# Performance work log

Hardware: AMD Instinct MI355X
Metric: run time of the kernel (lower is better)

## Reference

```python
import jax, jax.numpy as jnp
import numpy as np

B, T, E, H, M = 1, 2048, 1536, 16, 3
KVH = 8
NREP = H // KVH
HD = E // H // M  # 32
EPS = 1e-5


def setup_inputs() -> dict:
    key = jax.random.key(0)
    ks = jax.random.split(key, 6)
    x = jax.random.normal(ks[0], (B, T, E), jnp.float32)
    # true rotary tables: freqs = pos * 10000^{-2i/d}, shape [T, HD//2]
    inv_freq = 1.0 / (10000.0 ** (np.arange(0, HD, 2, dtype=np.float64) / HD))
    ang = np.outer(np.arange(T, dtype=np.float64), inv_freq)
    cos = jnp.asarray(np.cos(ang), jnp.float32)
    sin = jnp.asarray(np.sin(ang), jnp.float32)
    s = 0.02
    q_w = s * jax.random.normal(ks[1], (M, E // M, E), jnp.float32)
    k_w = s * jax.random.normal(ks[2], (M, E // M // NREP, E), jnp.float32)
    v_w = s * jax.random.normal(ks[3], (E // NREP, E), jnp.float32)
    out_w = s * jax.random.normal(ks[4], (E, E), jnp.float32)
    raw_map_weights = jnp.array([0.1, -0.1, 0.1], jnp.float32)
    weight_scale = jnp.ones((1,), jnp.float32)
    subln_w = jnp.ones((M * HD,), jnp.float32)
    return dict(x=x, cos=cos, sin=sin, q_w=q_w, k_w=k_w, v_w=v_w,
                out_w=out_w, raw_map_weights=raw_map_weights,
                weight_scale=weight_scale, subln_w=subln_w)


def _rope_interleaved(t, cos, sin):
    # t: [..., seq, heads, hd]; cos/sin: [seq, hd//2]
    x1 = t[..., 0::2]
    x2 = t[..., 1::2]
    c = cos[:, None, :]
    s = sin[:, None, :]
    o1 = x1 * c - x2 * s
    o2 = x1 * s + x2 * c
    return jnp.stack([o1, o2], axis=-1).reshape(t.shape)


def reference(x, cos, sin, q_w, k_w, v_w, out_w, raw_map_weights, weight_scale, subln_w):
    b, t, e = x.shape
    m = q_w.shape[0]
    hd = 2 * cos.shape[-1]
    h = q_w.shape[1] // hd
    kvh = k_w.shape[1] // hd
    nrep = h // kvh
    scaling = hd ** -0.5

    map_w = jnp.tanh(raw_map_weights) * weight_scale  # [M]

    # per-map Q/K projections, all maps at once
    q = jnp.einsum('bte,mfe->mbtf', x, q_w).reshape(m, b, t, h, hd)
    k = jnp.einsum('bte,mfe->mbtf', x, k_w).reshape(m, b, t, kvh, hd)
    q = _rope_interleaved(q, cos, sin) * scaling
    k = _rope_interleaved(k, cos, sin)
    q = q.transpose(0, 1, 3, 2, 4)                      # [m,b,h,t,hd]
    k = jnp.repeat(k.transpose(0, 1, 3, 2, 4), nrep, axis=2)  # [m,b,h,t,hd]

    v = jnp.einsum('bte,fe->btf', x, v_w).reshape(b, t, kvh, m * hd)
    v = jnp.repeat(v.transpose(0, 2, 1, 3), nrep, axis=1)  # [b,h,t,m*hd]

    causal = jnp.where(jnp.triu(jnp.ones((t, t), bool), 1),
                       jnp.float32(-jnp.inf), jnp.float32(0.0))

    scores = jnp.einsum('mbhtd,mbhsd->mbhts', q, k)
    scores = jnp.nan_to_num(scores) + causal
    attn_w = jax.nn.softmax(scores.astype(jnp.float32), axis=-1).astype(x.dtype)
    combined = jnp.einsum('m,mbhts->bhts', map_w, attn_w)

    attn = jnp.einsum('bhts,bhsf->bhtf', combined, v)  # [b,h,t,m*hd]
    # RMSNorm over last dim
    var = jnp.mean(jnp.square(attn.astype(jnp.float32)), axis=-1, keepdims=True)
    attn = (attn * jax.lax.rsqrt(var + EPS)).astype(attn.dtype) * subln_w

    attn = attn.transpose(0, 2, 1, 3).reshape(b, t, h * m * hd)
    return jnp.einsum('bte,fe->btf', attn, out_w)
```

## Files before the change

kernel.cpp:

```cpp
#include <hip/hip_runtime.h>
#include <hip/hip_bf16.h>
#include <math.h>

#define T_DIM 2048
#define E_DIM 1536
#define K_DIM 1536

typedef unsigned short u16;
typedef unsigned int u32;
typedef __attribute__((ext_vector_type(8))) short bf16x8;
typedef __attribute__((ext_vector_type(4))) float f32x4;

__device__ __forceinline__ u16 f2bf(float x) {
    unsigned u = __float_as_uint(x);
    return (u16)((u + 0x7fffu + ((u >> 16) & 1u)) >> 16);
}

#define GLOAD16(gsrc, ldst)                                                              \
    __builtin_amdgcn_global_load_lds((const __attribute__((address_space(1))) u32*)(gsrc), \
                                     (__attribute__((address_space(3))) u32*)(ldst), 16, 0, 0)

__global__ __launch_bounds__(256) void cvt_bf16_5(const float* __restrict__ s0, u16* __restrict__ d0,
                                                  const float* __restrict__ s1, u16* __restrict__ d1,
                                                  const float* __restrict__ s2, u16* __restrict__ d2,
                                                  const float* __restrict__ s3, u16* __restrict__ d3,
                                                  const float* __restrict__ s4, u16* __restrict__ d4) {
    int i = blockIdx.x * 256 + threadIdx.x;
    const float* s;
    u16* d;
    int off;
    if (i < 786432)       { s = s0; d = d0; off = i; }
    else if (i < 1376256) { s = s1; d = d1; off = i - 786432; }
    else if (i < 1671168) { s = s2; d = d2; off = i - 1376256; }
    else if (i < 1966080) { s = s3; d = d3; off = i - 1671168; }
    else                  { s = s4; d = d4; off = i - 1966080; }
    float4 v = ((const float4*)s)[off];
    ((ushort4*)d)[off] = make_ushort4(f2bf(v.x), f2bf(v.y), f2bf(v.z), f2bf(v.w));
}

__global__ __launch_bounds__(256) void gemm_qkv_fused(const u16* __restrict__ A,
                                                      const u16* __restrict__ W,
                                                      const float* __restrict__ cosb,
                                                      const float* __restrict__ sinb,
                                                      u16* __restrict__ qb16,
                                                      u16* __restrict__ kpack,
                                                      u16* __restrict__ vpack,
                                                      float qscale) {
    const int K = K_DIM;
    __shared__ __align__(16) u16 As[128 * 64];
    __shared__ __align__(16) u16 Bs[128 * 64];
    const int tid = threadIdx.x;
    const int lane = tid & 63;
    const int wv = tid >> 6;
    const int wr = wv >> 1;
    const int wc = wv & 1;
    const int cl = lane & 15;
    const int g = lane >> 4;
    const int bm = blockIdx.y * 128;
    const int bn = blockIdx.x * 128;

    const char* Ab = (const char*)A;
    const char* Wb = (const char*)W;

    size_t a_src[4], b_src[4];
    int dst[4];
#pragma unroll
    for (int is = 0; is < 4; ++is) {
        int b = is * 4096 + tid * 16;
        int row = b >> 7;
        int wi = b & 127;
        dst[is] = b;
        a_src[is] = (size_t)(bm + row) * (K * 2) + (wi ^ ((row & 7) << 4));
        b_src[is] = (size_t)(bn + row) * (K * 2) + (wi ^ ((row & 7) << 4));
    }

    f32x4 acc[4][4];
#pragma unroll
    for (int mi = 0; mi < 4; ++mi)
#pragma unroll
        for (int ni = 0; ni < 4; ++ni) acc[mi][ni] = (f32x4){0.f, 0.f, 0.f, 0.f};

    for (int k0b = 0; k0b < K * 2; k0b += 128) {
#pragma unroll
        for (int is = 0; is < 4; ++is)
            GLOAD16(Ab + a_src[is] + k0b, (char*)As + dst[is]);
#pragma unroll
        for (int is = 0; is < 4; ++is)
            GLOAD16(Wb + b_src[is] + k0b, (char*)Bs + dst[is]);
        __syncthreads();
#pragma unroll
        for (int kk = 0; kk < 2; ++kk) {
            const int co = (kk * 64 + g * 16) ^ ((cl & 7) << 4);
            bf16x8 af[4], bfr[4];
#pragma unroll
            for (int mi = 0; mi < 4; ++mi)
                af[mi] = *(const bf16x8*)((const char*)As + (wr * 64 + mi * 16 + cl) * 128 + co);
#pragma unroll
            for (int ni = 0; ni < 4; ++ni)
                bfr[ni] = *(const bf16x8*)((const char*)Bs + (wc * 64 + ni * 16 + cl) * 128 + co);
#pragma unroll
            for (int mi = 0; mi < 4; ++mi)
#pragma unroll
                for (int ni = 0; ni < 4; ++ni)
                    acc[mi][ni] = __builtin_amdgcn_mfma_f32_16x16x32_bf16(af[mi], bfr[ni], acc[mi][ni], 0, 0, 0);
        }
        __syncthreads();
    }

    if (bn < 1536) {
#pragma unroll
        for (int mi = 0; mi < 4; ++mi)
#pragma unroll
            for (int ni = 0; ni < 4; ++ni)
#pragma unroll
                for (int r = 0; r < 4; ++r) {
                    int trow = bm + wr * 64 + mi * 16 + 4 * g + r;
                    int c = bn + wc * 64 + ni * 16 + cl;
                    float v = acc[mi][ni][r];
                    float pv = __shfl_xor(v, 1, 64);
                    int i = (c & 31) >> 1;
                    float cs = cosb[trow * 16 + i];
                    float sn = sinb[trow * 16 + i];
                    float o = v * cs + ((c & 1) ? pv * sn : -pv * sn);
                    qb16[(size_t)trow * E_DIM + c] = f2bf(o * qscale);
                }
    } else if (bn < 2304) {
#pragma unroll
        for (int mi = 0; mi < 4; ++mi)
#pragma unroll
            for (int ni = 0; ni < 4; ++ni)
#pragma unroll
                for (int r = 0; r < 4; ++r) {
                    int trow = bm + wr * 64 + mi * 16 + 4 * g + r;
                    int c = bn + wc * 64 + ni * 16 + cl;
                    float v = acc[mi][ni][r];
                    float pv = __shfl_xor(v, 1, 64);
                    int i = (c & 31) >> 1;
                    float cs = cosb[trow * 16 + i];
                    float sn = sinb[trow * 16 + i];
                    float o = v * cs + ((c & 1) ? pv * sn : -pv * sn);
                    int ck = c - 1536;
                    int m = ck >> 8;
                    int rem = ck & 255;
                    int kvhh = rem >> 5;
                    int d = rem & 31;
                    int cch = trow >> 5, st2 = (trow >> 4) & 1, colk = trow & 15;
                    size_t dstb = ((((size_t)(kvhh * 64 + cch) * 3 + m) * 2 + st2) * 16 + colk) * 32 + d;
                    kpack[dstb] = f2bf(o);
                }
    } else {
#pragma unroll
        for (int mi = 0; mi < 4; ++mi)
#pragma unroll
            for (int ni = 0; ni < 4; ++ni)
#pragma unroll
                for (int r = 0; r < 4; ++r) {
                    int trow = bm + wr * 64 + mi * 16 + 4 * g + r;
                    int c = bn + wc * 64 + ni * 16 + cl;
                    int fq = c - 2304;
                    int kvhh = fq / 96;
                    int f = fq - kvhh * 96;
                    size_t dstb = ((size_t)(kvhh * 64 + (trow >> 5)) * 96 + f) * 32 + (trow & 31);
                    vpack[dstb] = f2bf(acc[mi][ni][r]);
                }
    }
}

__global__ __launch_bounds__(256) void gemm_mfma_out(const u16* __restrict__ A,
                                                     const u16* __restrict__ W,
                                                     float* __restrict__ Cp,
                                                     int K, int ldC) {
    __shared__ __align__(16) u16 As[128 * 64];
    __shared__ __align__(16) u16 Bs[64 * 64];
    const int tid = threadIdx.x;
    const int lane = tid & 63;
    const int wv = tid >> 6;
    const int wr = wv >> 1;
    const int wc = wv & 1;
    const int cl = lane & 15;
    const int g = lane >> 4;
    const int bm = blockIdx.y * 128;
    const int bn = blockIdx.x * 64;

    const char* Ab = (const char*)A;
    const char* Wb = (const char*)W;

    size_t a_src[4];
    int a_dst[4];
#pragma unroll
    for (int is = 0; is < 4; ++is) {
        int b = is * 4096 + wv * 1024 + lane * 16;
        int row = b >> 7;
        int wi = b & 127;
        a_src[is] = (size_t)(bm + row) * (K * 2) + (wi ^ ((row & 7) << 4));
        a_dst[is] = b;
    }
    size_t b_src[2];
    int b_dst[2];
#pragma unroll
    for (int is = 0; is < 2; ++is) {
        int b = is * 4096 + wv * 1024 + lane * 16;
        int row = b >> 7;
        int wi = b & 127;
        b_src[is] = (size_t)(bn + row) * (K * 2) + (wi ^ ((row & 7) << 4));
        b_dst[is] = b;
    }

    f32x4 acc[4][2];
#pragma unroll
    for (int mi = 0; mi < 4; ++mi)
#pragma unroll
        for (int ni = 0; ni < 2; ++ni) acc[mi][ni] = (f32x4){0.f, 0.f, 0.f, 0.f};

    for (int k0b = 0; k0b < K * 2; k0b += 128) {
#pragma unroll
        for (int is = 0; is < 4; ++is)
            GLOAD16(Ab + a_src[is] + k0b, (char*)As + a_dst[is]);
#pragma unroll
        for (int is = 0; is < 2; ++is)
            GLOAD16(Wb + b_src[is] + k0b, (char*)Bs + b_dst[is]);
        __syncthreads();
#pragma unroll
        for (int kk = 0; kk < 2; ++kk) {
            const int co = (kk * 64 + g * 16) ^ ((cl & 7) << 4);
            bf16x8 af[4], bfr[2];
#pragma unroll
            for (int mi = 0; mi < 4; ++mi)
                af[mi] = *(const bf16x8*)((const char*)As + (wr * 64 + mi * 16 + cl) * 128 + co);
#pragma unroll
            for (int ni = 0; ni < 2; ++ni)
                bfr[ni] = *(const bf16x8*)((const char*)Bs + (wc * 32 + ni * 16 + cl) * 128 + co);
#pragma unroll
            for (int mi = 0; mi < 4; ++mi)
#pragma unroll
                for (int ni = 0; ni < 2; ++ni)
                    acc[mi][ni] = __builtin_amdgcn_mfma_f32_16x16x32_bf16(af[mi], bfr[ni], acc[mi][ni], 0, 0, 0);
        }
        __syncthreads();
    }

#pragma unroll
    for (int mi = 0; mi < 4; ++mi)
#pragma unroll
        for (int ni = 0; ni < 2; ++ni)
#pragma unroll
            for (int r = 0; r < 4; ++r) {
                size_t row = bm + wr * 64 + mi * 16 + 4 * g + r;
                size_t col = bn + wc * 32 + ni * 16 + cl;
                Cp[row * ldC + col] = acc[mi][ni][r];
            }
}

__global__ __launch_bounds__(384) void attn_one(const u16* __restrict__ qb,
                                                const u16* __restrict__ kpack,
                                                const u16* __restrict__ vpack,
                                                const float* __restrict__ raw_map,
                                                const float* __restrict__ wscale,
                                                const float* __restrict__ subln,
                                                u16* __restrict__ outb) {
    __shared__ __align__(16) char smem[36864];
    const int tid = threadIdx.x;
    const int lane = tid & 63;
    const int wv = tid >> 6;
    const int m = wv >> 1;
    const int ks = wv & 1;
    const int col = lane & 15;
    const int g = lane >> 4;
    const int lid = blockIdx.y * 64 + blockIdx.x;
    const int kvh = lid & 7;
    const int rest = lid >> 3;
    const int h = kvh * 2 + (rest & 1);
    const int qt = 63 - (rest >> 1);
    const int qbase = qt * 32;
    const int nfull = qt;

    u16 (*plds)[2][16][48] = (u16(*)[2][16][48])smem;
    float (*red1)[2][16] = (float(*)[2][16])smem;

    bf16x8 qfrag[2];
#pragma unroll
    for (int q2 = 0; q2 < 2; ++q2)
        qfrag[q2] = *(const bf16x8*)(qb + (size_t)(qbase + 16 * q2 + col) * E_DIM + m * 512 + h * 32 + 8 * g);

    f32x4 oacc[2][6];
#pragma unroll
    for (int q2 = 0; q2 < 2; ++q2)
#pragma unroll
        for (int ft = 0; ft < 6; ++ft) oacc[q2][ft] = (f32x4){0.f, 0.f, 0.f, 0.f};
    float lsum[2] = {0.f, 0.f};

    const int laneoff = col * 32 + 8 * g;
    const u16* kt = kpack + ((size_t)(kvh * 64 + ks) * 3 + m) * 1024 + laneoff;
    const u16* vt = vpack + (size_t)(kvh * 64 + ks) * 3072 + laneoff;

    for (int c = ks; c < nfull; c += 2) {
        bf16x8 kf0 = *(const bf16x8*)(kt);
        bf16x8 kf1 = *(const bf16x8*)(kt + 512);
        bf16x8 vf[6];
#pragma unroll
        for (int u = 0; u < 6; ++u) vf[u] = *(const bf16x8*)(vt + u * 512);
        kt += 2 * 3072;
        vt += 2 * 3072;

        __builtin_amdgcn_s_setprio(1);
#pragma unroll
        for (int q2 = 0; q2 < 2; ++q2) {
            f32x4 sv0 = __builtin_amdgcn_mfma_f32_16x16x32_bf16(kf0, qfrag[q2], (f32x4){0.f, 0.f, 0.f, 0.f}, 0, 0, 0);
            f32x4 sv1 = __builtin_amdgcn_mfma_f32_16x16x32_bf16(kf1, qfrag[q2], (f32x4){0.f, 0.f, 0.f, 0.f}, 0, 0, 0);
            float p0 = __builtin_amdgcn_exp2f(sv0[0]);
            float p1 = __builtin_amdgcn_exp2f(sv0[1]);
            float p2 = __builtin_amdgcn_exp2f(sv0[2]);
            float p3 = __builtin_amdgcn_exp2f(sv0[3]);
            float p4 = __builtin_amdgcn_exp2f(sv1[0]);
            float p5 = __builtin_amdgcn_exp2f(sv1[1]);
            float p6 = __builtin_amdgcn_exp2f(sv1[2]);
            float p7 = __builtin_amdgcn_exp2f(sv1[3]);
            lsum[q2] += ((p0 + p1) + (p2 + p3)) + ((p4 + p5) + (p6 + p7));
            __hip_bfloat162 a01 = __float22bfloat162_rn(make_float2(p0, p1));
            __hip_bfloat162 a23 = __float22bfloat162_rn(make_float2(p2, p3));
            __hip_bfloat162 b01 = __float22bfloat162_rn(make_float2(p4, p5));
            __hip_bfloat162 b23 = __float22bfloat162_rn(make_float2(p6, p7));
            uint2 w0, w1;
            w0.x = *(u32*)&a01; w0.y = *(u32*)&a23;
            w1.x = *(u32*)&b01; w1.y = *(u32*)&b23;
            *(uint2*)&plds[wv][q2][col][4 * g] = w0;
            *(uint2*)&plds[wv][q2][col][16 + 4 * g] = w1;
        }
#pragma unroll
        for (int q2 = 0; q2 < 2; ++q2) {
            bf16x8 pf = *(const bf16x8*)&plds[wv][q2][col][8 * g];
#pragma unroll
            for (int ft = 0; ft < 6; ++ft)
                oacc[q2][ft] = __builtin_amdgcn_mfma_f32_16x16x32_bf16(pf, vf[ft], oacc[q2][ft], 0, 0, 0);
        }
        __builtin_amdgcn_s_setprio(0);
    }

    if ((nfull & 1) == ks) {
        const u16* ktm = kpack + ((size_t)(kvh * 64 + nfull) * 3 + m) * 1024 + laneoff;
        const u16* vtm = vpack + (size_t)(kvh * 64 + nfull) * 3072 + laneoff;
        bf16x8 kf0 = *(const bf16x8*)(ktm);
        bf16x8 kf1 = *(const bf16x8*)(ktm + 512);
        bf16x8 vf[6];
#pragma unroll
        for (int u = 0; u < 6; ++u) vf[u] = *(const bf16x8*)(vtm + u * 512);

        {
            f32x4 sv = __builtin_amdgcn_mfma_f32_16x16x32_bf16(kf0, qfrag[0], (f32x4){0.f, 0.f, 0.f, 0.f}, 0, 0, 0);
            float p[4];
#pragma unroll
            for (int r = 0; r < 4; ++r) {
                float x = (4 * g + r > col) ? -1e30f : sv[r];
                p[r] = __builtin_amdgcn_exp2f(x);
                lsum[0] += p[r];
            }
            __hip_bfloat162 a01 = __float22bfloat162_rn(make_float2(p[0], p[1]));
            __hip_bfloat162 a23 = __float22bfloat162_rn(make_float2(p[2], p[3]));
            uint2 w0;
            w0.x = *(u32*)&a01; w0.y = *(u32*)&a23;
            *(uint2*)&plds[wv][0][col][4 * g] = w0;
            uint2 z = make_uint2(0u, 0u);
            *(uint2*)&plds[wv][0][col][16 + 4 * g] = z;
        }
        {
            f32x4 sv0 = __builtin_amdgcn_mfma_f32_16x16x32_bf16(kf0, qfrag[1], (f32x4){0.f, 0.f, 0.f, 0.f}, 0, 0, 0);
            f32x4 sv1 = __builtin_amdgcn_mfma_f32_16x16x32_bf16(kf1, qfrag[1], (f32x4){0.f, 0.f, 0.f, 0.f}, 0, 0, 0);
            float p0[4], p1[4];
#pragma unroll
            for (int r = 0; r < 4; ++r) {
                p0[r] = __builtin_amdgcn_exp2f(sv0[r]);
                float x = (4 * g + r > col) ? -1e30f : sv1[r];
                p1[r] = __builtin_amdgcn_exp2f(x);
                lsum[1] += p0[r] + p1[r];
            }
            __hip_bfloat162 a01 = __float22bfloat162_rn(make_float2(p0[0], p0[1]));
            __hip_bfloat162 a23 = __float22bfloat162_rn(make_float2(p0[2], p0[3]));
            __hip_bfloat162 b01 = __float22bfloat162_rn(make_float2(p1[0], p1[1]));
            __hip_bfloat162 b23 = __float22bfloat162_rn(make_float2(p1[2], p1[3]));
            uint2 w0, w1;
            w0.x = *(u32*)&a01; w0.y = *(u32*)&a23;
            w1.x = *(u32*)&b01; w1.y = *(u32*)&b23;
            *(uint2*)&plds[wv][1][col][4 * g] = w0;
            *(uint2*)&plds[wv][1][col][16 + 4 * g] = w1;
        }
#pragma unroll
        for (int q2 = 0; q2 < 2; ++q2) {
            bf16x8 pf = *(const bf16x8*)&plds[wv][q2][col][8 * g];
#pragma unroll
            for (int ft = 0; ft < 6; ++ft)
                oacc[q2][ft] = __builtin_amdgcn_mfma_f32_16x16x32_bf16(pf, vf[ft], oacc[q2][ft], 0, 0, 0);
        }
    }

#pragma unroll
    for (int q2 = 0; q2 < 2; ++q2) {
        lsum[q2] += __shfl_xor(lsum[q2], 16, 64);
        lsum[q2] += __shfl_xor(lsum[q2], 32, 64);
    }
    __syncthreads();
    if (g == 0) {
#pragma unroll
        for (int q2 = 0; q2 < 2; ++q2) red1[wv][q2][col] = lsum[q2];
    }
    __syncthreads();

    {
        float mwm = tanhf(raw_map[m]) * wscale[0];
#pragma unroll
        for (int q2 = 0; q2 < 2; ++q2)
#pragma unroll
            for (int r = 0; r < 4; ++r) {
                float tot = red1[2 * m][q2][4 * g + r] + red1[2 * m + 1][q2][4 * g + r];
                float f = mwm / tot;
                oacc[q2][0][r] *= f; oacc[q2][1][r] *= f; oacc[q2][2][r] *= f;
                oacc[q2][3][r] *= f; oacc[q2][4][r] *= f; oacc[q2][5][r] *= f;
            }
    }
    __syncthreads();

    float* redA = (float*)smem;
    if (wv >= 3) {
        float4* rp = (float4*)(redA + (size_t)(wv - 3) * 3072 + (size_t)lane * 48);
#pragma unroll
        for (int q2 = 0; q2 < 2; ++q2)
#pragma unroll
            for (int ft = 0; ft < 6; ++ft)
                rp[q2 * 6 + ft] = make_float4(oacc[q2][ft][0], oacc[q2][ft][1], oacc[q2][ft][2], oacc[q2][ft][3]);
    }
    __syncthreads();
    if (wv < 3) {
        const float4* rp = (const float4*)(redA + (size_t)wv * 3072 + (size_t)lane * 48);
#pragma unroll
        for (int q2 = 0; q2 < 2; ++q2)
#pragma unroll
            for (int ft = 0; ft < 6; ++ft) {
                float4 a = rp[q2 * 6 + ft];
                oacc[q2][ft][0] += a.x; oacc[q2][ft][1] += a.y;
                oacc[q2][ft][2] += a.z; oacc[q2][ft][3] += a.w;
            }
    }
    __syncthreads();
    if (wv == 1 || wv == 2) {
        float4* rp = (float4*)(redA + (size_t)(wv - 1) * 3072 + (size_t)lane * 48);
#pragma unroll
        for (int q2 = 0; q2 < 2; ++q2)
#pragma unroll
            for (int ft = 0; ft < 6; ++ft)
                rp[q2 * 6 + ft] = make_float4(oacc[q2][ft][0], oacc[q2][ft][1], oacc[q2][ft][2], oacc[q2][ft][3]);
    }
    __syncthreads();
    if (wv != 0) return;
#pragma unroll
    for (int s2 = 0; s2 < 2; ++s2) {
        const float4* rp = (const float4*)(redA + (size_t)s2 * 3072 + (size_t)lane * 48);
#pragma unroll
        for (int q2 = 0; q2 < 2; ++q2)
#pragma unroll
            for (int ft = 0; ft < 6; ++ft) {
                float4 a = rp[q2 * 6 + ft];
                oacc[q2][ft][0] += a.x; oacc[q2][ft][1] += a.y;
                oacc[q2][ft][2] += a.z; oacc[q2][ft][3] += a.w;
            }
    }

    float ss[2][4] = {{0.f, 0.f, 0.f, 0.f}, {0.f, 0.f, 0.f, 0.f}};
#pragma unroll
    for (int q2 = 0; q2 < 2; ++q2)
#pragma unroll
        for (int ft = 0; ft < 6; ++ft)
#pragma unroll
            for (int r = 0; r < 4; ++r) ss[q2][r] += oacc[q2][ft][r] * oacc[q2][ft][r];
#pragma unroll
    for (int q2 = 0; q2 < 2; ++q2)
#pragma unroll
        for (int r = 0; r < 4; ++r) {
            ss[q2][r] += __shfl_xor(ss[q2][r], 1, 64);
            ss[q2][r] += __shfl_xor(ss[q2][r], 2, 64);
            ss[q2][r] += __shfl_xor(ss[q2][r], 4, 64);
            ss[q2][r] += __shfl_xor(ss[q2][r], 8, 64);
            ss[q2][r] = rsqrtf(ss[q2][r] * (1.f / 96.f) + 1e-5f);
        }
#pragma unroll
    for (int ft = 0; ft < 6; ++ft) {
        float sl = subln[ft * 16 + col];
#pragma unroll
        for (int q2 = 0; q2 < 2; ++q2)
#pragma unroll
            for (int r = 0; r < 4; ++r) {
                int trow = qbase + 16 * q2 + 4 * g + r;
                outb[(size_t)trow * E_DIM + h * 96 + ft * 16 + col] = f2bf(oacc[q2][ft][r] * ss[q2][r] * sl);
            }
    }
}

extern "C" void kernel_launch(void* const* d_in, const int* in_sizes, int n_in,
                              void* d_out, int out_size, void* d_ws, size_t ws_size,
                              hipStream_t stream) {
    const float* x       = (const float*)d_in[0];
    const float* cosb    = (const float*)d_in[1];
    const float* sinb    = (const float*)d_in[2];
    const float* q_w     = (const float*)d_in[3];
    const float* k_w     = (const float*)d_in[4];
    const float* v_w     = (const float*)d_in[5];
    const float* out_w   = (const float*)d_in[6];
    const float* raw_map = (const float*)d_in[7];
    const float* wscale  = (const float*)d_in[8];
    const float* subln   = (const float*)d_in[9];
    float* out = (float*)d_out;

    char* ws = (char*)d_ws;
    u16* xb16   = (u16*)(ws);
    u16* wqkv16 = (u16*)(ws + 6291456);
    u16* qb16   = (u16*)(ws + 15728640);
    u16* kpack  = (u16*)(ws + 22020096);
    u16* vpack  = (u16*)(ws + 25190400);
    u16* wout16 = (u16*)(ws + 28360704);
    u16* ab16   = xb16;

    cvt_bf16_5<<<9984, 256, 0, stream>>>(x, xb16,
                                         q_w, wqkv16,
                                         k_w, wqkv16 + 2359296,
                                         v_w, wqkv16 + 3538944,
                                         out_w, wout16);

    const float qscale = 0.17677669529663687f * 1.4426950408889634f;
    gemm_qkv_fused<<<dim3(3072 / 128, T_DIM / 128), 256, 0, stream>>>(
        xb16, wqkv16, cosb, sinb, qb16, kpack, vpack, qscale);

    attn_one<<<dim3(64, 16), 384, 0, stream>>>(qb16, kpack, vpack, raw_map, wscale, subln, ab16);

    gemm_mfma_out<<<dim3(E_DIM / 64, T_DIM / 128), 256, 0, stream>>>(ab16, wout16, out, K_DIM, E_DIM);
}
```

Baseline: 133.7 us.

## Repartition attention waves by query half instead of map to shrink reduction

The attention kernel moves from 6 waves (3 maps × 2 key splits) to 4 waves (2 query halves × 2 key splits). Each wave now handles all three maps for 16 query rows and reuses its V fragments across them. The map-weighted combine happens in registers, so the cross-wave output reduction drops from a multi-stage LDS reduction over 6 waves to a single exchange. The trade-off is higher register pressure (18 accumulator tiles, 12 K/V fragments) and fewer waves per block, which may lower occupancy and latency hiding.

```diff
diff --git a/kernel.cpp b/kernel.cpp
--- a/kernel.cpp
+++ b/kernel.cpp
@@ -251,19 +251,19 @@
             }
 }
 
-__global__ __launch_bounds__(384) void attn_one(const u16* __restrict__ qb,
-                                                const u16* __restrict__ kpack,
-                                                const u16* __restrict__ vpack,
-                                                const float* __restrict__ raw_map,
-                                                const float* __restrict__ wscale,
-                                                const float* __restrict__ subln,
-                                                u16* __restrict__ outb) {
-    __shared__ __align__(16) char smem[36864];
+__global__ __launch_bounds__(256) void attn_fused(const u16* __restrict__ qb,
+                                                  const u16* __restrict__ kpack,
+                                                  const u16* __restrict__ vpack,
+                                                  const float* __restrict__ raw_map,
+                                                  const float* __restrict__ wscale,
+                                                  const float* __restrict__ subln,
+                                                  u16* __restrict__ outb) {
+    __shared__ __align__(16) char smem[15360];
     const int tid = threadIdx.x;
     const int lane = tid & 63;
     const int wv = tid >> 6;
-    const int m = wv >> 1;
-    const int ks = wv & 1;
+    const int q2 = wv & 1;
+    const int ks = wv >> 1;
     const int col = lane & 15;
     const int g = lane >> 4;
     const int lid = blockIdx.y * 64 + blockIdx.x;
@@ -274,222 +274,198 @@
     const int qbase = qt * 32;
     const int nfull = qt;
 
-    u16 (*plds)[2][16][48] = (u16(*)[2][16][48])smem;
-    float (*red1)[2][16] = (float(*)[2][16])smem;
-
-    bf16x8 qfrag[2];
-#pragma unroll
-    for (int q2 = 0; q2 < 2; ++q2)
-        qfrag[q2] = *(const bf16x8*)(qb + (size_t)(qbase + 16 * q2 + col) * E_DIM + m * 512 + h * 32 + 8 * g);
-
-    f32x4 oacc[2][6];
-#pragma unroll
-    for (int q2 = 0; q2 < 2; ++q2)
-#pragma unroll
-        for (int ft = 0; ft < 6; ++ft) oacc[q2][ft] = (f32x4){0.f, 0.f, 0.f, 0.f};
-    float lsum[2] = {0.f, 0.f};
+    u16 (*plds)[3][16][40] = (u16(*)[3][16][40])smem;
+    float (*red1)[3][16] = (float(*)[3][16])smem;
+    float (*red2)[64][28] = (float(*)[64][28])smem;
+
+    bf16x8 qfrag[3];
+#pragma unroll
+    for (int m = 0; m < 3; ++m)
+        qfrag[m] = *(const bf16x8*)(qb + (size_t)(qbase + 16 * q2 + col) * E_DIM + m * 512 + h * 32 + 8 * g);
+
+    f32x4 oacc[3][6];
+#pragma unroll
+    for (int m = 0; m < 3; ++m)
+#pragma unroll
+        for (int ft = 0; ft < 6; ++ft) oacc[m][ft] = (f32x4){0.f, 0.f, 0.f, 0.f};
+    float lsum[3] = {0.f, 0.f, 0.f};
 
     const int laneoff = col * 32 + 8 * g;
-    const u16* kt = kpack + ((size_t)(kvh * 64 + ks) * 3 + m) * 1024 + laneoff;
-    const u16* vt = vpack + (size_t)(kvh * 64 + ks) * 3072 + laneoff;
+    const u16* kt = kpack + (size_t)(kvh * 64 + ks) * 3072;
+    const u16* vt = vpack + (size_t)(kvh * 64 + ks) * 3072;
 
     for (int c = ks; c < nfull; c += 2) {
-        bf16x8 kf0 = *(const bf16x8*)(kt);
-        bf16x8 kf1 = *(const bf16x8*)(kt + 512);
-        bf16x8 vf[6];
-#pragma unroll
-        for (int u = 0; u < 6; ++u) vf[u] = *(const bf16x8*)(vt + u * 512);
+        bf16x8 kf[6], vf[6];
+#pragma unroll
+        for (int u = 0; u < 6; ++u) kf[u] = *(const bf16x8*)(kt + laneoff + u * 512);
+#pragma unroll
+        for (int u = 0; u < 6; ++u) vf[u] = *(const bf16x8*)(vt + laneoff + u * 512);
         kt += 2 * 3072;
         vt += 2 * 3072;
 
         __builtin_amdgcn_s_setprio(1);
 #pragma unroll
-        for (int q2 = 0; q2 < 2; ++q2) {
-            f32x4 sv0 = __builtin_amdgcn_mfma_f32_16x16x32_bf16(kf0, qfrag[q2], (f32x4){0.f, 0.f, 0.f, 0.f}, 0, 0, 0);
-            f32x4 sv1 = __builtin_amdgcn_mfma_f32_16x16x32_bf16(kf1, qfrag[q2], (f32x4){0.f, 0.f, 0.f, 0.f}, 0, 0, 0);
-            float p0 = __builtin_amdgcn_exp2f(sv0[0]);
-            float p1 = __builtin_amdgcn_exp2f(sv0[1]);
-            float p2 = __builtin_amdgcn_exp2f(sv0[2]);
-            float p3 = __builtin_amdgcn_exp2f(sv0[3]);
-            float p4 = __builtin_amdgcn_exp2f(sv1[0]);
-            float p5 = __builtin_amdgcn_exp2f(sv1[1]);
-            float p6 = __builtin_amdgcn_exp2f(sv1[2]);
-            float p7 = __builtin_amdgcn_exp2f(sv1[3]);
-            lsum[q2] += ((p0 + p1) + (p2 + p3)) + ((p4 + p5) + (p6 + p7));
-            __hip_bfloat162 a01 = __float22bfloat162_rn(make_float2(p0, p1));
-            __hip_bfloat162 a23 = __float22bfloat162_rn(make_float2(p2, p3));
-            __hip_bfloat162 b01 = __float22bfloat162_rn(make_float2(p4, p5));
-            __hip_bfloat162 b23 = __float22bfloat162_rn(make_float2(p6, p7));
-            uint2 w0, w1;
-            w0.x = *(u32*)&a01; w0.y = *(u32*)&a23;
-            w1.x = *(u32*)&b01; w1.y = *(u32*)&b23;
-            *(uint2*)&plds[wv][q2][col][4 * g] = w0;
-            *(uint2*)&plds[wv][q2][col][16 + 4 * g] = w1;
-        }
-#pragma unroll
-        for (int q2 = 0; q2 < 2; ++q2) {
-            bf16x8 pf = *(const bf16x8*)&plds[wv][q2][col][8 * g];
+        for (int m = 0; m < 3; ++m)
+#pragma unroll
+            for (int st = 0; st < 2; ++st) {
+                f32x4 sv = __builtin_amdgcn_mfma_f32_16x16x32_bf16(
+                    kf[m * 2 + st], qfrag[m], (f32x4){0.f, 0.f, 0.f, 0.f}, 0, 0, 0);
+                float p0 = __builtin_amdgcn_exp2f(sv[0]);
+                float p1 = __builtin_amdgcn_exp2f(sv[1]);
+                float p2 = __builtin_amdgcn_exp2f(sv[2]);
+                float p3 = __builtin_amdgcn_exp2f(sv[3]);
+                lsum[m] += (p0 + p1) + (p2 + p3);
+                __hip_bfloat162 b01 = __float22bfloat162_rn(make_float2(p0, p1));
+                __hip_bfloat162 b23 = __float22bfloat162_rn(make_float2(p2, p3));
+                uint2 w;
+                w.x = *(u32*)&b01;
+                w.y = *(u32*)&b23;
+                *(uint2*)&plds[wv][m][col][st * 16 + 4 * g] = w;
+            }
+#pragma unroll
+        for (int m = 0; m < 3; ++m) {
+            bf16x8 pf = *(const bf16x8*)&plds[wv][m][col][8 * g];
 #pragma unroll
             for (int ft = 0; ft < 6; ++ft)
-                oacc[q2][ft] = __builtin_amdgcn_mfma_f32_16x16x32_bf16(pf, vf[ft], oacc[q2][ft], 0, 0, 0);
+                oacc[m][ft] = __builtin_amdgcn_mfma_f32_16x16x32_bf16(pf, vf[ft], oacc[m][ft], 0, 0, 0);
         }
         __builtin_amdgcn_s_setprio(0);
     }
 
     if ((nfull & 1) == ks) {
-        const u16* ktm = kpack + ((size_t)(kvh * 64 + nfull) * 3 + m) * 1024 + laneoff;
+        const u16* ktm = kpack + (size_t)(kvh * 64 + nfull) * 3072 + laneoff;
         const u16* vtm = vpack + (size_t)(kvh * 64 + nfull) * 3072 + laneoff;
-        bf16x8 kf0 = *(const bf16x8*)(ktm);
-        bf16x8 kf1 = *(const bf16x8*)(ktm + 512);
-        bf16x8 vf[6];
+        bf16x8 kf[6], vf[6];
+#pragma unroll
+        for (int u = 0; u < 6; ++u) kf[u] = *(const bf16x8*)(ktm + u * 512);
 #pragma unroll
         for (int u = 0; u < 6; ++u) vf[u] = *(const bf16x8*)(vtm + u * 512);
 
-        {
-            f32x4 sv = __builtin_amdgcn_mfma_f32_16x16x32_bf16(kf0, qfrag[0], (f32x4){0.f, 0.f, 0.f, 0.f}, 0, 0, 0);
-            float p[4];
-#pragma unroll
-            for (int r = 0; r < 4; ++r) {
-                float x = (4 * g + r > col) ? -1e30f : sv[r];
-                p[r] = __builtin_amdgcn_exp2f(x);
-                lsum[0] += p[r];
+#pragma unroll
+        for (int m = 0; m < 3; ++m) {
+            if (q2 == 0) {
+                f32x4 sv = __builtin_amdgcn_mfma_f32_16x16x32_bf16(
+                    kf[m * 2 + 0], qfrag[m], (f32x4){0.f, 0.f, 0.f, 0.f}, 0, 0, 0);
+                float p[4];
+#pragma unroll
+                for (int r = 0; r < 4; ++r) {
+                    float x = (4 * g + r > col) ? -1e30f : sv[r];
+                    p[r] = __builtin_amdgcn_exp2f(x);
+                    lsum[m] += p[r];
+                }
+                __hip_bfloat162 a01 = __float22bfloat162_rn(make_float2(p[0], p[1]));
+                __hip_bfloat162 a23 = __float22bfloat162_rn(make_float2(p[2], p[3]));
+                uint2 w0;
+                w0.x = *(u32*)&a01; w0.y = *(u32*)&a23;
+                *(uint2*)&plds[wv][m][col][4 * g] = w0;
+                uint2 z = make_uint2(0u, 0u);
+                *(uint2*)&plds[wv][m][col][16 + 4 * g] = z;
+            } else {
+                f32x4 sv0 = __builtin_amdgcn_mfma_f32_16x16x32_bf16(
+                    kf[m * 2 + 0], qfrag[m], (f32x4){0.f, 0.f, 0.f, 0.f}, 0, 0, 0);
+                f32x4 sv1 = __builtin_amdgcn_mfma_f32_16x16x32_bf16(
+                    kf[m * 2 + 1], qfrag[m], (f32x4){0.f, 0.f, 0.f, 0.f}, 0, 0, 0);
+                float p0[4], p1[4];
+#pragma unroll
+                for (int r = 0; r < 4; ++r) {
+                    p0[r] = __builtin_amdgcn_exp2f(sv0[r]);
+                    float x = (4 * g + r > col) ? -1e30f : sv1[r];
+                    p1[r] = __builtin_amdgcn_exp2f(x);
+                    lsum[m] += p0[r] + p1[r];
+                }
+                __hip_bfloat162 a01 = __float22bfloat162_rn(make_float2(p0[0], p0[1]));
+                __hip_bfloat162 a23 = __float22bfloat162_rn(make_float2(p0[2], p0[3]));
+                __hip_bfloat162 b01 = __float22bfloat162_rn(make_float2(p1[0], p1[1]));
+                __hip_bfloat162 b23 = __float22bfloat162_rn(make_float2(p1[2], p1[3]));
+                uint2 w0, w1;
+                w0.x = *(u32*)&a01; w0.y = *(u32*)&a23;
+                w1.x = *(u32*)&b01; w1.y = *(u32*)&b23;
+                *(uint2*)&plds[wv][m][col][4 * g] = w0;
+                *(uint2*)&plds[wv][m][col][16 + 4 * g] = w1;
             }
-            __hip_bfloat162 a01 = __float22bfloat162_rn(make_float2(p[0], p[1]));
-            __hip_bfloat162 a23 = __float22bfloat162_rn(make_float2(p[2], p[3]));
-            uint2 w0;
-            w0.x = *(u32*)&a01; w0.y = *(u32*)&a23;
-            *(uint2*)&plds[wv][0][col][4 * g] = w0;
-            uint2 z = make_uint2(0u, 0u);
-            *(uint2*)&plds[wv][0][col][16 + 4 * g] = z;
-        }
-        {
-            f32x4 sv0 = __builtin_amdgcn_mfma_f32_16x16x32_bf16(kf0, qfrag[1], (f32x4){0.f, 0.f, 0.f, 0.f}, 0, 0, 0);
-            f32x4 sv1 = __builtin_amdgcn_mfma_f32_16x16x32_bf16(kf1, qfrag[1], (f32x4){0.f, 0.f, 0.f, 0.f}, 0, 0, 0);
-            float p0[4], p1[4];
-#pragma unroll
-            for (int r = 0; r < 4; ++r) {
-                p0[r] = __builtin_amdgcn_exp2f(sv0[r]);
-                float x = (4 * g + r > col) ? -1e30f : sv1[r];
-                p1[r] = __builtin_amdgcn_exp2f(x);
-                lsum[1] += p0[r] + p1[r];
-            }
-            __hip_bfloat162 a01 = __float22bfloat162_rn(make_float2(p0[0], p0[1]));
-            __hip_bfloat162 a23 = __float22bfloat162_rn(make_float2(p0[2], p0[3]));
-            __hip_bfloat162 b01 = __float22bfloat162_rn(make_float2(p1[0], p1[1]));
-            __hip_bfloat162 b23 = __float22bfloat162_rn(make_float2(p1[2], p1[3]));
-            uint2 w0, w1;
-            w0.x = *(u32*)&a01; w0.y = *(u32*)&a23;
-            w1.x = *(u32*)&b01; w1.y = *(u32*)&b23;
-            *(uint2*)&plds[wv][1][col][4 * g] = w0;
-            *(uint2*)&plds[wv][1][col][16 + 4 * g] = w1;
-        }
-#pragma unroll
-        for (int q2 = 0; q2 < 2; ++q2) {
-            bf16x8 pf = *(const bf16x8*)&plds[wv][q2][col][8 * g];
+        }
+#pragma unroll
+        for (int m = 0; m < 3; ++m) {
+            bf16x8 pf = *(const bf16x8*)&plds[wv][m][col][8 * g];
 #pragma unroll
             for (int ft = 0; ft < 6; ++ft)
-                oacc[q2][ft] = __builtin_amdgcn_mfma_f32_16x16x32_bf16(pf, vf[ft], oacc[q2][ft], 0, 0, 0);
-        }
-    }
-
-#pragma unroll
-    for (int q2 = 0; q2 < 2; ++q2) {
-        lsum[q2] += __shfl_xor(lsum[q2], 16, 64);
-        lsum[q2] += __shfl_xor(lsum[q2], 32, 64);
+                oacc[m][ft] = __builtin_amdgcn_mfma_f32_16x16x32_bf16(pf, vf[ft], oacc[m][ft], 0, 0, 0);
+        }
+    }
+
+#pragma unroll
+    for (int m = 0; m < 3; ++m) {
+        lsum[m] += __shfl_xor(lsum[m], 16, 64);
+        lsum[m] += __shfl_xor(lsum[m], 32, 64);
     }
     __syncthreads();
     if (g == 0) {
 #pragma unroll
-        for (int q2 = 0; q2 < 2; ++q2) red1[wv][q2][col] = lsum[q2];
+        for (int m = 0; m < 3; ++m) red1[wv][m][col] = lsum[m];
     }
     __syncthreads();
 
+    float facr[3][4];
     {
-        float mwm = tanhf(raw_map[m]) * wscale[0];
-#pragma unroll
-        for (int q2 = 0; q2 < 2; ++q2)
+        float wsc = wscale[0];
+#pragma unroll
+        for (int m = 0; m < 3; ++m) {
+            float mwm = tanhf(raw_map[m]) * wsc;
 #pragma unroll
             for (int r = 0; r < 4; ++r) {
-                float tot = red1[2 * m][q2][4 * g + r] + red1[2 * m + 1][q2][4 * g + r];
-                float f = mwm / tot;
-                oacc[q2][0][r] *= f; oacc[q2][1][r] *= f; oacc[q2][2][r] *= f;
-                oacc[q2][3][r] *= f; oacc[q2][4][r] *= f; oacc[q2][5][r] *= f;
+                float tot = red1[q2][m][4 * g + r] + red1[q2 + 2][m][4 * g + r];
+                facr[m][r] = mwm / tot;
             }
-    }
+        }
+    }
+
+    f32x4 occ[6];
+#pragma unroll
+    for (int ft = 0; ft < 6; ++ft)
+#pragma unroll
+        for (int r = 0; r < 4; ++r)
+            occ[ft][r] = facr[0][r] * oacc[0][ft][r] + facr[1][r] * oacc[1][ft][r] + facr[2][r] * oacc[2][ft][r];
+
     __syncthreads();
-
-    float* redA = (float*)smem;
-    if (wv >= 3) {
-        float4* rp = (float4*)(redA + (size_t)(wv - 3) * 3072 + (size_t)lane * 48);
-#pragma unroll
-        for (int q2 = 0; q2 < 2; ++q2)
-#pragma unroll
-            for (int ft = 0; ft < 6; ++ft)
-                rp[q2 * 6 + ft] = make_float4(oacc[q2][ft][0], oacc[q2][ft][1], oacc[q2][ft][2], oacc[q2][ft][3]);
+    if (ks == 1) {
+        float4* rp = (float4*)red2[q2][lane];
+#pragma unroll
+        for (int ft = 0; ft < 6; ++ft)
+            rp[ft] = make_float4(occ[ft][0], occ[ft][1], occ[ft][2], occ[ft][3]);
     }
     __syncthreads();
-    if (wv < 3) {
-        const float4* rp = (const float4*)(redA + (size_t)wv * 3072 + (size_t)lane * 48);
-#pragma unroll
-        for (int q2 = 0; q2 < 2; ++q2)
-#pragma unroll
-            for (int ft = 0; ft < 6; ++ft) {
-                float4 a = rp[q2 * 6 + ft];
-                oacc[q2][ft][0] += a.x; oacc[q2][ft][1] += a.y;
-                oacc[q2][ft][2] += a.z; oacc[q2][ft][3] += a.w;
-            }
-    }
-    __syncthreads();
-    if (wv == 1 || wv == 2) {
-        float4* rp = (float4*)(redA + (size_t)(wv - 1) * 3072 + (size_t)lane * 48);
-#pragma unroll
-        for (int q2 = 0; q2 < 2; ++q2)
-#pragma unroll
-            for (int ft = 0; ft < 6; ++ft)
-                rp[q2 * 6 + ft] = make_float4(oacc[q2][ft][0], oacc[q2][ft][1], oacc[q2][ft][2], oacc[q2][ft][3]);
-    }
-    __syncthreads();
-    if (wv != 0) return;
-#pragma unroll
-    for (int s2 = 0; s2 < 2; ++s2) {
-        const float4* rp = (const float4*)(redA + (size_t)s2 * 3072 + (size_t)lane * 48);
-#pragma unroll
-        for (int q2 = 0; q2 < 2; ++q2)
-#pragma unroll
-            for (int ft = 0; ft < 6; ++ft) {
-                float4 a = rp[q2 * 6 + ft];
-                oacc[q2][ft][0] += a.x; oacc[q2][ft][1] += a.y;
-                oacc[q2][ft][2] += a.z; oacc[q2][ft][3] += a.w;
-            }
-    }
-
-    float ss[2][4] = {{0.f, 0.f, 0.f, 0.f}, {0.f, 0.f, 0.f, 0.f}};
-#pragma unroll
-    for (int q2 = 0; q2 < 2; ++q2)
-#pragma unroll
-        for (int ft = 0; ft < 6; ++ft)
-#pragma unroll
-            for (int r = 0; r < 4; ++r) ss[q2][r] += oacc[q2][ft][r] * oacc[q2][ft][r];
-#pragma unroll
-    for (int q2 = 0; q2 < 2; ++q2)
-#pragma unroll
-        for (int r = 0; r < 4; ++r) {
-            ss[q2][r] += __shfl_xor(ss[q2][r], 1, 64);
-            ss[q2][r] += __shfl_xor(ss[q2][r], 2, 64);
-            ss[q2][r] += __shfl_xor(ss[q2][r], 4, 64);
-            ss[q2][r] += __shfl_xor(ss[q2][r], 8, 64);
-            ss[q2][r] = rsqrtf(ss[q2][r] * (1.f / 96.f) + 1e-5f);
-        }
+    if (ks != 0) return;
+    {
+        const float4* rp = (const float4*)red2[q2][lane];
+#pragma unroll
+        for (int ft = 0; ft < 6; ++ft) {
+            float4 a = rp[ft];
+            occ[ft][0] += a.x; occ[ft][1] += a.y;
+            occ[ft][2] += a.z; occ[ft][3] += a.w;
+        }
+    }
+
+    float ss[4] = {0.f, 0.f, 0.f, 0.f};
+#pragma unroll
+    for (int ft = 0; ft < 6; ++ft)
+#pragma unroll
+        for (int r = 0; r < 4; ++r) ss[r] += occ[ft][r] * occ[ft][r];
+#pragma unroll
+    for (int r = 0; r < 4; ++r) {
+        ss[r] += __shfl_xor(ss[r], 1, 64);
+        ss[r] += __shfl_xor(ss[r], 2, 64);
+        ss[r] += __shfl_xor(ss[r], 4, 64);
+        ss[r] += __shfl_xor(ss[r], 8, 64);
+        ss[r] = rsqrtf(ss[r] * (1.f / 96.f) + 1e-5f);
+    }
 #pragma unroll
     for (int ft = 0; ft < 6; ++ft) {
         float sl = subln[ft * 16 + col];
 #pragma unroll
-        for (int q2 = 0; q2 < 2; ++q2)
-#pragma unroll
-            for (int r = 0; r < 4; ++r) {
-                int trow = qbase + 16 * q2 + 4 * g + r;
-                outb[(size_t)trow * E_DIM + h * 96 + ft * 16 + col] = f2bf(oacc[q2][ft][r] * ss[q2][r] * sl);
-            }
+        for (int r = 0; r < 4; ++r) {
+            int trow = qbase + 16 * q2 + 4 * g + r;
+            outb[(size_t)trow * E_DIM + h * 96 + ft * 16 + col] = f2bf(occ[ft][r] * ss[r] * sl);
+        }
     }
 }
 
@@ -527,7 +503,7 @@
     gemm_qkv_fused<<<dim3(3072 / 128, T_DIM / 128), 256, 0, stream>>>(
         xb16, wqkv16, cosb, sinb, qb16, kpack, vpack, qscale);
 
-    attn_one<<<dim3(64, 16), 384, 0, stream>>>(qb16, kpack, vpack, raw_map, wscale, subln, ab16);
+    attn_fused<<<dim3(64, 16), 256, 0, stream>>>(qb16, kpack, vpack, raw_map, wscale, subln, ab16);
 
     gemm_mfma_out<<<dim3(E_DIM / 64, T_DIM / 128), 256, 0, stream>>>(ab16, wout16, out, K_DIM, E_DIM);
 }
```

Measured after the change: 129.2 us. -3.3%, faster.
